# Performance work log

Measured on AMD Instinct MI355X. Metric: run time of the kernel, lower is better.

## Reference

```python
import jax, jax.numpy as jnp
import numpy as np

NEG_INF = jnp.finfo(jnp.float32).min


def _continual_mask(attach_test_after, Q, K, test_num, chunk_size):
    """Boolean allowed-mask [B, 1, Q, K] replicating get_continual_mask +
    the per-batch test-query/train-key override in forward()."""
    k_train = K - test_num * chunk_size
    q_train = Q - test_num * chunk_size
    qi = jnp.arange(Q)[:, None]          # [Q,1]
    kj = jnp.arange(K)[None, :]          # [1,K]
    # base causal mask with diagonal offset K-Q (train queries)
    base = kj <= qi + (K - Q)            # [Q,K]
    # block-diagonal tril for test-query / test-key region
    dq = qi - q_train                    # local test row (negative for train rows, unused there)
    dk = kj - k_train
    block = (kj >= k_train) & (dk <= dq) & ((dk // chunk_size) == (dq // chunk_size))
    # per-batch: test query in chunk n may see train keys <= attach_test_after[b, n]
    chunk_idx = jnp.clip(dq[:, 0], 0, None) // chunk_size          # [Q]
    att = attach_test_after[:, chunk_idx]                          # [B,Q]
    train_key_allowed = kj[None, :, :] <= att[:, :, None]          # [B,Q,K]
    allowed = jnp.where(qi < q_train, base[None],
                        jnp.where(kj[None] < k_train, train_key_allowed, block[None]))
    return allowed[:, None]              # [B,1,Q,K]


def setup_inputs() -> dict:
    key = jax.random.key(0)
    k1, k2, k3, k4 = jax.random.split(key, 4)
    B, L, H, D = 4, 2048, 8, 64
    test_num, train_len = 64, 1536
    return {
        "queries": jax.random.normal(k1, (B, L, H, D), dtype=jnp.float32),
        "keys": jax.random.normal(k2, (B, L, H, D), dtype=jnp.float32),
        "values": jax.random.normal(k3, (B, L, H, D), dtype=jnp.float32),
        "attach_test_after": jax.random.randint(k4, (B, test_num), 0, train_len).astype(jnp.int64),
        "train_len": train_len,
    }


def reference(queries, keys, values, attach_test_after, train_len):
    B, Lq, H, Dqk = queries.shape
    test_num = attach_test_after.shape[1]
    chunk_size = (Lq - train_len) // test_num
    q = jnp.transpose(queries, (0, 2, 1, 3))   # [B,H,Lq,D]
    k = jnp.transpose(keys, (0, 2, 1, 3))      # [B,H,Lk,D]
    v = jnp.transpose(values, (0, 2, 1, 3))    # [B,H,Lk,Dv]
    Lk = k.shape[2]
    # vanilla path: scaled QK^T + continual mask + softmax + AV
    logits = jnp.einsum('bhmd,bhnd->bhmn', q, k) / jnp.sqrt(jnp.float32(Dqk))
    allowed = _continual_mask(attach_test_after, Lq, Lk, test_num, chunk_size)
    logits = jnp.where(allowed, logits, NEG_INF)
    attn = jax.nn.softmax(logits, axis=-1)
    out = jnp.einsum('bhmn,bhnd->bhmd', attn, v)
    return out.transpose(0, 2, 1, 3).reshape(B, Lq, H * v.shape[-1])  # b l (h d)
```

## Files before the change

### kernel.cpp

```cpp
#include <hip/hip_runtime.h>
#include <hip/hip_bf16.h>

typedef __bf16 bf16_t;
typedef __bf16 bf16x8 __attribute__((ext_vector_type(8)));
typedef float  f32x4  __attribute__((ext_vector_type(4)));

#define MFMA16(a, b, c) __builtin_amdgcn_mfma_f32_16x16x32_bf16((a), (b), (c), 0, 0, 0)

constexpr int Bc = 4, Lc = 2048, Hc = 8, Dc = 64;
constexpr int HD = Hc * Dc;
constexpr int TRAINc = 1536;
constexpr int ROWS_BLK = 64;
constexpr int KT = 32;
constexpr int PSTR = 40;

__global__ void prep_k(const float* __restrict__ K, bf16_t* __restrict__ Kb) {
  size_t g = ((size_t)blockIdx.x * 256 + threadIdx.x) * 8;
  float4 a = *(const float4*)(K + g);
  float4 b = *(const float4*)(K + g + 4);
  bf16x8 v;
  v[0] = (bf16_t)a.x; v[1] = (bf16_t)a.y; v[2] = (bf16_t)a.z; v[3] = (bf16_t)a.w;
  v[4] = (bf16_t)b.x; v[5] = (bf16_t)b.y; v[6] = (bf16_t)b.z; v[7] = (bf16_t)b.w;
  *(bf16x8*)(Kb + g) = v;
}

__global__ void prep_v(const float* __restrict__ V, bf16_t* __restrict__ Vt) {
  __shared__ bf16_t T[64][72];
  const int bid = blockIdx.x;
  const int kt = bid & 31, h = (bid >> 5) & 7, b = bid >> 8;
  const int t = (int)threadIdx.x;
  {
    int kl = t >> 2, dp = (t & 3) << 4;
    const float* s = V + ((size_t)(b * Lc + kt * 64 + kl) * Hc + h) * Dc + dp;
    bf16x8 v0, v1;
    float4 f;
    f = *(const float4*)(s);      v0[0]=(bf16_t)f.x; v0[1]=(bf16_t)f.y; v0[2]=(bf16_t)f.z; v0[3]=(bf16_t)f.w;
    f = *(const float4*)(s + 4);  v0[4]=(bf16_t)f.x; v0[5]=(bf16_t)f.y; v0[6]=(bf16_t)f.z; v0[7]=(bf16_t)f.w;
    f = *(const float4*)(s + 8);  v1[0]=(bf16_t)f.x; v1[1]=(bf16_t)f.y; v1[2]=(bf16_t)f.z; v1[3]=(bf16_t)f.w;
    f = *(const float4*)(s + 12); v1[4]=(bf16_t)f.x; v1[5]=(bf16_t)f.y; v1[6]=(bf16_t)f.z; v1[7]=(bf16_t)f.w;
    *(bf16x8*)&T[kl][dp] = v0;
    *(bf16x8*)&T[kl][dp + 8] = v1;
  }
  __syncthreads();
  {
    int d = t >> 2, kp = (t & 3) << 4;
    bf16x8 o0, o1;
#pragma unroll
    for (int i = 0; i < 8; ++i) { o0[i] = T[kp + i][d]; o1[i] = T[kp + 8 + i][d]; }
    bf16_t* dst = Vt + ((size_t)((b * Hc + h) * Dc + d)) * Lc + kt * 64 + kp;
    *(bf16x8*)dst = o0;
    *(bf16x8*)(dst + 8) = o1;
  }
}

static __device__ __forceinline__ void load16(const bf16_t* g, bf16_t* l) {
  __builtin_amdgcn_global_load_lds(
      (const __attribute__((address_space(1))) unsigned int*)g,
      (__attribute__((address_space(3))) unsigned int*)l, 16, 0, 0);
}

__global__ __launch_bounds__(256, 2)
void continual_attn(const float* __restrict__ Qg, const bf16_t* __restrict__ Kb,
                    const bf16_t* __restrict__ Vt, const int* __restrict__ ATT,
                    float* __restrict__ OUT)
{
  __shared__ __align__(16) bf16_t Klds[KT * 64];
  __shared__ __align__(16) bf16_t Vlds[Dc * KT];
  __shared__ __align__(16) bf16_t Plds[4][16 * PSTR];

  const int bid  = blockIdx.x;
  const int qblk = bid & 31;
  const int h    = (bid >> 5) & 7;
  const int b    = bid >> 8;
  const int q0   = qblk * ROWS_BLK;

  const int tid  = (int)threadIdx.x;
  const int wave = tid >> 6;
  const int lane = tid & 63;
  const int quad = lane >> 4;
  const int col  = lane & 15;
  const int qw   = q0 + wave * 16;

  const size_t bhQ = (size_t)b * Lc * HD + (size_t)h * Dc;

  const int kr = tid >> 3;
  const int kc = (tid & 7) ^ (kr & 7);
  const bf16_t* ksrc0 = Kb + bhQ + (size_t)kr * HD + kc * 8;
  const int vd = tid >> 2;
  const bf16_t* vsrc0 = Vt + ((size_t)((b * Hc + h) * Dc + vd)) * Lc + (tid & 3) * 8;
  bf16_t* kdst = &Klds[wave * 512];
  bf16_t* vdst = &Vlds[wave * 512];

  bf16x8 aq[2];
  {
    const float* qp = Qg + bhQ + (size_t)(qw + col) * HD + quad * 8;
#pragma unroll
    for (int t = 0; t < 2; ++t) {
      float4 lo = *(const float4*)(qp + t * 32);
      float4 hi = *(const float4*)(qp + t * 32 + 4);
      bf16x8 v;
      v[0] = (bf16_t)(lo.x * 0.125f); v[1] = (bf16_t)(lo.y * 0.125f);
      v[2] = (bf16_t)(lo.z * 0.125f); v[3] = (bf16_t)(lo.w * 0.125f);
      v[4] = (bf16_t)(hi.x * 0.125f); v[5] = (bf16_t)(hi.y * 0.125f);
      v[6] = (bf16_t)(hi.z * 0.125f); v[7] = (bf16_t)(hi.w * 0.125f);
      aq[t] = v;
    }
  }

  const bool testblk = (q0 >= TRAINc);
  int kend[4], cstart[4], qir[4];
#pragma unroll
  for (int r = 0; r < 4; ++r) {
    int qi = qw + quad * 4 + r;
    qir[r] = qi;
    if (testblk) {
      kend[r]   = ATT[b * 64 + ((qi - TRAINc) >> 3)] + 1;
      cstart[r] = qi & ~7;
    } else {
      kend[r]   = qi + 1;
      cstart[r] = 0;
    }
  }

  int ntA, ndiag, kfull_end;
  if (testblk) {
    int c0 = (q0 - TRAINc) >> 3;
    int amax = 0, amin = 0x7fffffff;
#pragma unroll
    for (int i = 0; i < 8; ++i) {
      int a = ATT[b * 64 + c0 + i];
      amax = (a > amax) ? a : amax;
      amin = (a < amin) ? a : amin;
    }
    ntA = (amax >> 5) + 1;
    ndiag = 2;
    kfull_end = amin + 1;
  } else {
    ntA = (q0 >> 5) + 2;
    ndiag = 0;
    kfull_end = q0 + 1;
  }
  const int ntot = ntA + ndiag;

  float lsumL[4] = {0.f, 0.f, 0.f, 0.f};
  f32x4 o0 = {0,0,0,0}, o1 = {0,0,0,0}, o2 = {0,0,0,0}, o3 = {0,0,0,0};

  for (int ti = 0; ti < ntot; ++ti) {
    const int k0 = (ti < ntA) ? ti * KT : q0 + (ti - ntA) * KT;

    __syncthreads();
    load16(ksrc0 + (size_t)k0 * HD, kdst);
    load16(vsrc0 + k0, vdst);
    __syncthreads();

    f32x4 s0 = {0,0,0,0}, s1 = {0,0,0,0};
    {
      const int cs = col & 7;
      const int cA = (quad ^ cs) << 3;
      const int cB = ((4 + quad) ^ cs) << 3;
      bf16x8 b00 = *(const bf16x8*)&Klds[col * 64 + cA];
      bf16x8 b01 = *(const bf16x8*)&Klds[col * 64 + cB];
      bf16x8 b10 = *(const bf16x8*)&Klds[(16 + col) * 64 + cA];
      bf16x8 b11 = *(const bf16x8*)&Klds[(16 + col) * 64 + cB];
      s0 = MFMA16(aq[0], b00, s0);
      s0 = MFMA16(aq[1], b01, s0);
      s1 = MFMA16(aq[0], b10, s1);
      s1 = MFMA16(aq[1], b11, s1);
    }

    float sv0[4], sv1[4];
#pragma unroll
    for (int r = 0; r < 4; ++r) { sv0[r] = s0[r]; sv1[r] = s1[r]; }

    const int mode = (ti >= ntA) ? 2 : ((k0 + KT <= kfull_end) ? 0 : 1);
    if (mode == 1) {
      const int c0g = k0 + col, c1g = k0 + 16 + col;
#pragma unroll
      for (int r = 0; r < 4; ++r) {
        if (c0g >= kend[r]) sv0[r] = -1e30f;
        if (c1g >= kend[r]) sv1[r] = -1e30f;
      }
    } else if (mode == 2) {
      const int c0g = k0 + col, c1g = k0 + 16 + col;
#pragma unroll
      for (int r = 0; r < 4; ++r) {
        if (c0g < cstart[r] || c0g > qir[r]) sv0[r] = -1e30f;
        if (c1g < cstart[r] || c1g > qir[r]) sv1[r] = -1e30f;
      }
    }

    bf16_t* pw = Plds[wave];
#pragma unroll
    for (int r = 0; r < 4; ++r) {
      float p0 = __expf(sv0[r]);
      float p1 = __expf(sv1[r]);
      lsumL[r] += p0 + p1;
      pw[(quad * 4 + r) * PSTR + col]      = (bf16_t)p0;
      pw[(quad * 4 + r) * PSTR + 16 + col] = (bf16_t)p1;
    }
    bf16x8 pa = *(const bf16x8*)&pw[col * PSTR + quad * 8];

#pragma unroll
    for (int t = 0; t < 4; ++t) {
      bf16x8 vb = *(const bf16x8*)&Vlds[(t * 16 + col) * KT + quad * 8];
      if      (t == 0) o0 = MFMA16(pa, vb, o0);
      else if (t == 1) o1 = MFMA16(pa, vb, o1);
      else if (t == 2) o2 = MFMA16(pa, vb, o2);
      else             o3 = MFMA16(pa, vb, o3);
    }
  }

#pragma unroll
  for (int r = 0; r < 4; ++r) {
    float rs = lsumL[r];
    rs += __shfl_xor(rs, 1);
    rs += __shfl_xor(rs, 2);
    rs += __shfl_xor(rs, 4);
    rs += __shfl_xor(rs, 8);
    float inv = 1.f / rs;
    int qi = qw + quad * 4 + r;
    float* op = OUT + ((size_t)b * Lc + qi) * HD + (size_t)h * Dc + col;
    op[0]  = o0[r] * inv;
    op[16] = o1[r] * inv;
    op[32] = o2[r] * inv;
    op[48] = o3[r] * inv;
  }
}

extern "C" void kernel_launch(void* const* d_in, const int* in_sizes, int n_in,
                              void* d_out, int out_size, void* d_ws, size_t ws_size,
                              hipStream_t stream) {
  const float* Q   = (const float*)d_in[0];
  const float* K   = (const float*)d_in[1];
  const float* V   = (const float*)d_in[2];
  const int*   ATT = (const int*)d_in[3];
  float* OUT = (float*)d_out;
  (void)in_sizes; (void)n_in; (void)out_size; (void)ws_size;

  const size_t NE = (size_t)Bc * Lc * Hc * Dc;
  bf16_t* Kb = (bf16_t*)d_ws;
  bf16_t* Vt = Kb + NE;

  prep_k<<<dim3((unsigned)(NE / 8 / 256)), dim3(256), 0, stream>>>(K, Kb);
  prep_v<<<dim3(Bc * Hc * (Lc / 64)), dim3(256), 0, stream>>>(V, Vt);
  continual_attn<<<dim3(Bc * Hc * (Lc / ROWS_BLK)), dim3(256), 0, stream>>>(Q, Kb, Vt, ATT, OUT);
}
```

Before: 148.6 us.

## Double-buffer 64-key K/V tiles with async LDS prefetch and heavy-first block order

```diff
diff --git a/kernel.cpp b/kernel.cpp
--- a/kernel.cpp
+++ b/kernel.cpp
@@ -11,8 +11,8 @@
 constexpr int HD = Hc * Dc;
 constexpr int TRAINc = 1536;
 constexpr int ROWS_BLK = 64;
-constexpr int KT = 32;
-constexpr int PSTR = 40;
+constexpr int KT = 64;
+constexpr int PST = 72;
 
 __global__ void prep_k(const float* __restrict__ K, bf16_t* __restrict__ Kb) {
   size_t g = ((size_t)blockIdx.x * 256 + threadIdx.x) * 8;
@@ -64,14 +64,14 @@
                     const bf16_t* __restrict__ Vt, const int* __restrict__ ATT,
                     float* __restrict__ OUT)
 {
-  __shared__ __align__(16) bf16_t Klds[KT * 64];
-  __shared__ __align__(16) bf16_t Vlds[Dc * KT];
-  __shared__ __align__(16) bf16_t Plds[4][16 * PSTR];
+  __shared__ __align__(16) bf16_t Klds[2][KT * 64];
+  __shared__ __align__(16) bf16_t Vlds[2][Dc * KT];
+  __shared__ __align__(16) bf16_t Plds[4][16 * PST];
 
   const int bid  = blockIdx.x;
-  const int qblk = bid & 31;
-  const int h    = (bid >> 5) & 7;
-  const int b    = bid >> 8;
+  const int qblk = 31 - (bid >> 5);
+  const int h    = bid & 7;
+  const int b    = (bid >> 3) & 3;
   const int q0   = qblk * ROWS_BLK;
 
   const int tid  = (int)threadIdx.x;
@@ -84,12 +84,9 @@
   const size_t bhQ = (size_t)b * Lc * HD + (size_t)h * Dc;
 
   const int kr = tid >> 3;
-  const int kc = (tid & 7) ^ (kr & 7);
-  const bf16_t* ksrc0 = Kb + bhQ + (size_t)kr * HD + kc * 8;
-  const int vd = tid >> 2;
-  const bf16_t* vsrc0 = Vt + ((size_t)((b * Hc + h) * Dc + vd)) * Lc + (tid & 3) * 8;
-  bf16_t* kdst = &Klds[wave * 512];
-  bf16_t* vdst = &Vlds[wave * 512];
+  const bf16_t* ksrcA = Kb + bhQ + (size_t)kr * HD + (((tid & 7) ^ (kr & 7)) << 3);
+  const bf16_t* vsrcA = Vt + ((size_t)((b * Hc + h) * Dc + kr)) * Lc + (((tid & 7) ^ (kr & 7)) << 3);
+  const bf16_t* vsrcB = vsrcA + (size_t)32 * Lc;
 
   bf16x8 aq[2];
   {
@@ -132,81 +129,97 @@
       amax = (a > amax) ? a : amax;
       amin = (a < amin) ? a : amin;
     }
-    ntA = (amax >> 5) + 1;
-    ndiag = 2;
+    ntA = (amax >> 6) + 1;
+    ndiag = 1;
     kfull_end = amin + 1;
   } else {
-    ntA = (q0 >> 5) + 2;
+    ntA = qblk + 1;
     ndiag = 0;
     kfull_end = q0 + 1;
   }
   const int ntot = ntA + ndiag;
 
   float lsumL[4] = {0.f, 0.f, 0.f, 0.f};
-  f32x4 o0 = {0,0,0,0}, o1 = {0,0,0,0}, o2 = {0,0,0,0}, o3 = {0,0,0,0};
+  f32x4 o[4] = {{0,0,0,0},{0,0,0,0},{0,0,0,0},{0,0,0,0}};
+
+  const int cA = ((quad ^ (col & 7)) << 3);
+
+  {
+    bf16_t* kd = Klds[0];
+    bf16_t* vd = Vlds[0];
+    load16(ksrcA, kd + wave * 512);
+    load16(ksrcA + (size_t)32 * HD, kd + 2048 + wave * 512);
+    load16(vsrcA, vd + wave * 512);
+    load16(vsrcB, vd + 2048 + wave * 512);
+  }
 
   for (int ti = 0; ti < ntot; ++ti) {
+    const int buf = ti & 1;
+    __syncthreads();
+
+    if (ti + 1 < ntot) {
+      const int kn = (ti + 1 < ntA) ? (ti + 1) * KT : q0 + (ti + 1 - ntA) * KT;
+      bf16_t* kd = Klds[1 - buf];
+      bf16_t* vd = Vlds[1 - buf];
+      load16(ksrcA + (size_t)kn * HD, kd + wave * 512);
+      load16(ksrcA + (size_t)(kn + 32) * HD, kd + 2048 + wave * 512);
+      load16(vsrcA + kn, vd + wave * 512);
+      load16(vsrcB + kn, vd + 2048 + wave * 512);
+    }
+
+    const bf16_t* kb = Klds[buf];
+    const bf16_t* vbuf = Vlds[buf];
     const int k0 = (ti < ntA) ? ti * KT : q0 + (ti - ntA) * KT;
 
-    __syncthreads();
-    load16(ksrc0 + (size_t)k0 * HD, kdst);
-    load16(vsrc0 + k0, vdst);
-    __syncthreads();
-
-    f32x4 s0 = {0,0,0,0}, s1 = {0,0,0,0};
-    {
-      const int cs = col & 7;
-      const int cA = (quad ^ cs) << 3;
-      const int cB = ((4 + quad) ^ cs) << 3;
-      bf16x8 b00 = *(const bf16x8*)&Klds[col * 64 + cA];
-      bf16x8 b01 = *(const bf16x8*)&Klds[col * 64 + cB];
-      bf16x8 b10 = *(const bf16x8*)&Klds[(16 + col) * 64 + cA];
-      bf16x8 b11 = *(const bf16x8*)&Klds[(16 + col) * 64 + cB];
-      s0 = MFMA16(aq[0], b00, s0);
-      s0 = MFMA16(aq[1], b01, s0);
-      s1 = MFMA16(aq[0], b10, s1);
-      s1 = MFMA16(aq[1], b11, s1);
-    }
-
-    float sv0[4], sv1[4];
-#pragma unroll
-    for (int r = 0; r < 4; ++r) { sv0[r] = s0[r]; sv1[r] = s1[r]; }
+    f32x4 sf[4] = {{0,0,0,0},{0,0,0,0},{0,0,0,0},{0,0,0,0}};
+#pragma unroll
+    for (int kg = 0; kg < 4; ++kg) {
+      const bf16_t* krow = kb + (kg * 16 + col) * 64;
+      bf16x8 k0f = *(const bf16x8*)(krow + cA);
+      bf16x8 k1f = *(const bf16x8*)(krow + (cA ^ 32));
+      sf[kg] = MFMA16(aq[0], k0f, sf[kg]);
+      sf[kg] = MFMA16(aq[1], k1f, sf[kg]);
+    }
 
     const int mode = (ti >= ntA) ? 2 : ((k0 + KT <= kfull_end) ? 0 : 1);
     if (mode == 1) {
-      const int c0g = k0 + col, c1g = k0 + 16 + col;
-#pragma unroll
-      for (int r = 0; r < 4; ++r) {
-        if (c0g >= kend[r]) sv0[r] = -1e30f;
-        if (c1g >= kend[r]) sv1[r] = -1e30f;
+#pragma unroll
+      for (int kg = 0; kg < 4; ++kg) {
+        const int kgv = k0 + kg * 16 + col;
+#pragma unroll
+        for (int r = 0; r < 4; ++r)
+          if (kgv >= kend[r]) sf[kg][r] = -1e30f;
       }
     } else if (mode == 2) {
-      const int c0g = k0 + col, c1g = k0 + 16 + col;
+#pragma unroll
+      for (int kg = 0; kg < 4; ++kg) {
+        const int kgv = k0 + kg * 16 + col;
+#pragma unroll
+        for (int r = 0; r < 4; ++r)
+          if (kgv < cstart[r] || kgv > qir[r]) sf[kg][r] = -1e30f;
+      }
+    }
+
+    bf16_t* pw = Plds[wave];
+#pragma unroll
+    for (int kg = 0; kg < 4; ++kg) {
 #pragma unroll
       for (int r = 0; r < 4; ++r) {
-        if (c0g < cstart[r] || c0g > qir[r]) sv0[r] = -1e30f;
-        if (c1g < cstart[r] || c1g > qir[r]) sv1[r] = -1e30f;
+        float p = __expf(sf[kg][r]);
+        lsumL[r] += p;
+        pw[(quad * 4 + r) * PST + kg * 16 + col] = (bf16_t)p;
       }
     }
-
-    bf16_t* pw = Plds[wave];
-#pragma unroll
-    for (int r = 0; r < 4; ++r) {
-      float p0 = __expf(sv0[r]);
-      float p1 = __expf(sv1[r]);
-      lsumL[r] += p0 + p1;
-      pw[(quad * 4 + r) * PSTR + col]      = (bf16_t)p0;
-      pw[(quad * 4 + r) * PSTR + 16 + col] = (bf16_t)p1;
-    }
-    bf16x8 pa = *(const bf16x8*)&pw[col * PSTR + quad * 8];
+    bf16x8 pa0 = *(const bf16x8*)&pw[col * PST + quad * 8];
+    bf16x8 pa1 = *(const bf16x8*)&pw[col * PST + 32 + quad * 8];
 
 #pragma unroll
     for (int t = 0; t < 4; ++t) {
-      bf16x8 vb = *(const bf16x8*)&Vlds[(t * 16 + col) * KT + quad * 8];
-      if      (t == 0) o0 = MFMA16(pa, vb, o0);
-      else if (t == 1) o1 = MFMA16(pa, vb, o1);
-      else if (t == 2) o2 = MFMA16(pa, vb, o2);
-      else             o3 = MFMA16(pa, vb, o3);
+      const bf16_t* vrow = vbuf + (t * 16 + col) * 64;
+      bf16x8 v0 = *(const bf16x8*)(vrow + cA);
+      bf16x8 v1 = *(const bf16x8*)(vrow + (cA ^ 32));
+      o[t] = MFMA16(pa0, v0, o[t]);
+      o[t] = MFMA16(pa1, v1, o[t]);
     }
   }
 
@@ -220,10 +233,10 @@
     float inv = 1.f / rs;
     int qi = qw + quad * 4 + r;
     float* op = OUT + ((size_t)b * Lc + qi) * HD + (size_t)h * Dc + col;
-    op[0]  = o0[r] * inv;
-    op[16] = o1[r] * inv;
-    op[32] = o2[r] * inv;
-    op[48] = o3[r] * inv;
+    op[0]  = o[0][r] * inv;
+    op[16] = o[1][r] * inv;
+    op[32] = o[2][r] * inv;
+    op[48] = o[3][r] * inv;
   }
 }
 
```

Result: faster. 131.5 us (-11.5%).
